# Kernel tuning notes

Hardware: AMD Instinct MI355X
Metric: run time of the kernel (lower is better)

Reference implementation:

```python
import jax, jax.numpy as jnp
import numpy as np

B, C, H, W = 32, 3, 224, 224
P = 16
D = 768
HEADS, DH = 12, 64
INNER = HEADS * DH          # 768
DEPTH = 12
NUM_CLASSES = 1000
NP_ = (H // P) * (W // P)   # 196 patches
N = NP_ + 1                 # with cls token
PATCH_DIM = C * P * P       # 768
EPS = 1e-5


def _ln(x, g, b):
    mu = jnp.mean(x, axis=-1, keepdims=True)
    var = jnp.var(x, axis=-1, keepdims=True)
    return (x - mu) * jax.lax.rsqrt(var + EPS) * g + b


def setup_inputs() -> dict:
    key = jax.random.key(0)
    ks = jax.random.split(key, 16)
    s = 0.02
    return {
        "img": jax.random.normal(ks[0], (B, C, H, W), jnp.float32),
        "sph_dist": jax.random.uniform(ks[1], (N, N), jnp.float32),
        "patch_ln_g": jnp.ones((PATCH_DIM,), jnp.float32),
        "patch_ln_b": jnp.zeros((PATCH_DIM,), jnp.float32),
        "W_patch": jax.random.normal(ks[2], (PATCH_DIM, D), jnp.float32) * s,
        "b_patch": jnp.zeros((D,), jnp.float32),
        "emb_ln_g": jnp.ones((D,), jnp.float32),
        "emb_ln_b": jnp.zeros((D,), jnp.float32),
        "pos_emb": jax.random.normal(ks[3], (1, N, D), jnp.float32),
        "cls_tok": jax.random.normal(ks[4], (1, 1, D), jnp.float32),
        "ln_g": jnp.ones((DEPTH, D), jnp.float32),
        "ln_b": jnp.zeros((DEPTH, D), jnp.float32),
        "W_qkv": jax.random.normal(ks[5], (DEPTH, D, 3 * INNER), jnp.float32) * s,
        "W_out": jax.random.normal(ks[6], (DEPTH, INNER, D), jnp.float32) * s,
        "b_out": jnp.zeros((DEPTH, D), jnp.float32),
        "final_ln_g": jnp.ones((D,), jnp.float32),
        "final_ln_b": jnp.zeros((D,), jnp.float32),
        "W_head": jax.random.normal(ks[7], (D, NUM_CLASSES), jnp.float32) * s,
        "b_head": jnp.zeros((NUM_CLASSES,), jnp.float32),
    }


def _patchify(img):
    b = img.shape[0]
    # 'b c (h p1) (w p2) -> b (h w) (p1 p2 c)'
    x = img.reshape(b, C, H // P, P, W // P, P)
    x = x.transpose(0, 2, 4, 3, 5, 1)  # b h w p1 p2 c
    return x.reshape(b, NP_, PATCH_DIM)


def _attn_layer(x, sph_dist, g, bln, Wqkv, Wout, bout):
    b, n, _ = x.shape
    xn = _ln(x, g, bln)
    qkv = xn @ Wqkv                                  # [b,n,3*inner]
    q, k, v = jnp.split(qkv, 3, axis=-1)
    def heads(t):
        return t.reshape(b, n, HEADS, DH).transpose(0, 2, 1, 3)  # b h n d
    q, k, v = heads(q), heads(k), heads(v)
    dots = jnp.einsum('bhid,bhjd->bhij', q, k) * (DH ** -0.5)
    dw = dots * (1.0 + sph_dist)                     # broadcast over b,h
    mu = jnp.mean(dw, axis=1, keepdims=True)
    sd = jnp.std(dw, axis=1, keepdims=True, ddof=1)  # torch.std is unbiased
    dw = (dw - mu) / sd
    attn = jax.nn.softmax(dw, axis=-1)
    o = jnp.einsum('bhij,bhjd->bhid', attn, v)
    o = o.transpose(0, 2, 1, 3).reshape(b, n, INNER)
    return o @ Wout + bout


def reference(img, sph_dist, patch_ln_g, patch_ln_b, W_patch, b_patch,
              emb_ln_g, emb_ln_b, pos_emb, cls_tok,
              ln_g, ln_b, W_qkv, W_out, b_out,
              final_ln_g, final_ln_b, W_head, b_head):
    b = img.shape[0]
    x = _patchify(img)
    x = _ln(x, patch_ln_g, patch_ln_b)
    x = x @ W_patch + b_patch
    x = _ln(x, emb_ln_g, emb_ln_b)                   # [b, 196, D]
    cls = jnp.broadcast_to(cls_tok, (b, 1, D))
    x = jnp.concatenate([cls, x], axis=1)            # [b, 197, D]
    x = x + pos_emb[:, :x.shape[1]]
    for i in range(DEPTH):
        x = _attn_layer(x, sph_dist, ln_g[i], ln_b[i], W_qkv[i], W_out[i], b_out[i]) + x
    x = _ln(x, final_ln_g, final_ln_b)
    x = x[:, 0]                                      # cls pooling
    return x @ W_head + b_head
```

## Files before the change

kernel.cpp:

```cpp
#include <hip/hip_runtime.h>
#include <math.h>

constexpr int Bc = 32, Cch = 3, Hh = 224, Ww = 224, Pp = 16;
constexpr int Dd = 768, NH = 12, DHd = 64, INNERc = 768;
constexpr int DEPTHc = 12, NCLS = 1000;
constexpr int NPc = 196, Nn = 197, PD = 768;
constexpr float EPSf = 1e-5f;

typedef _Float16 half_t;
typedef __attribute__((ext_vector_type(8))) _Float16 half8;
typedef __attribute__((ext_vector_type(4))) float f32x4;
typedef __attribute__((ext_vector_type(4))) unsigned int uint32x4;

__device__ __forceinline__ float wave_red_sum(float v) {
#pragma unroll
    for (int m = 32; m; m >>= 1) v += __shfl_xor(v, m);
    return v;
}

__device__ __forceinline__ void block_red2(float& s, float& s2, float* red) {
    s = wave_red_sum(s);
    s2 = wave_red_sum(s2);
    int wid = threadIdx.x >> 6, lane = threadIdx.x & 63;
    if (lane == 0) { red[wid] = s; red[4 + wid] = s2; }
    __syncthreads();
    s = red[0] + red[1] + red[2] + red[3];
    s2 = red[4] + red[5] + red[6] + red[7];
}

__global__ __launch_bounds__(256) void k_patch_ln(
        const float* __restrict__ img, const float* __restrict__ g,
        const float* __restrict__ bb, half_t* __restrict__ out) {
    int pid = blockIdx.x;
    int b = pid / NPc, n = pid % NPc;
    int ph = n / 14, pw = n % 14;
    int t = threadIdx.x;
    __shared__ float red[8];
    float v[3];
#pragma unroll
    for (int i = 0; i < 3; i++) {
        int d = t + i * 256;
        int c = d % 3, q = (d / 3) & 15, p = d / 48;
        v[i] = img[((long)(b * Cch + c) * Hh + ph * Pp + p) * Ww + pw * Pp + q];
    }
    float s = v[0] + v[1] + v[2];
    float s2 = v[0] * v[0] + v[1] * v[1] + v[2] * v[2];
    block_red2(s, s2, red);
    float mu = s * (1.f / PD);
    float var = s2 * (1.f / PD) - mu * mu;
    float r = rsqrtf(var + EPSf);
#pragma unroll
    for (int i = 0; i < 3; i++) {
        int d = t + i * 256;
        out[(long)pid * PD + d] = (half_t)((v[i] - mu) * r * g[d] + bb[d]);
    }
}

template <typename T>
__global__ __launch_bounds__(256) void k_ln(
        const float* __restrict__ in, const float* __restrict__ g,
        const float* __restrict__ bb, T* __restrict__ out,
        long in_stride, long out_stride) {
    long row = blockIdx.x;
    const float* ip = in + row * in_stride;
    T* op = out + row * out_stride;
    int t = threadIdx.x;
    __shared__ float red[8];
    float v[3];
#pragma unroll
    for (int i = 0; i < 3; i++) v[i] = ip[t + i * 256];
    float s = v[0] + v[1] + v[2];
    float s2 = v[0] * v[0] + v[1] * v[1] + v[2] * v[2];
    block_red2(s, s2, red);
    float mu = s * (1.f / Dd);
    float var = s2 * (1.f / Dd) - mu * mu;
    float r = rsqrtf(var + EPSf);
#pragma unroll
    for (int i = 0; i < 3; i++) {
        int d = t + i * 256;
        op[d] = (T)((v[i] - mu) * r * g[d] + bb[d]);
    }
}

__global__ __launch_bounds__(256) void k_embed(
        const float* __restrict__ tmp, const float* __restrict__ cls,
        const float* __restrict__ pos, const float* __restrict__ g,
        const float* __restrict__ bb, float* __restrict__ x) {
    int pid = blockIdx.x;
    int b = pid / Nn, n = pid % Nn;
    int t = threadIdx.x;
    float* xp = x + (long)pid * Dd;
    if (n == 0) {
#pragma unroll
        for (int i = 0; i < 3; i++) {
            int d = t + i * 256;
            xp[d] = cls[d] + pos[d];
        }
        return;
    }
    const float* ip = tmp + (long)(b * NPc + n - 1) * Dd;
    __shared__ float red[8];
    float v[3];
#pragma unroll
    for (int i = 0; i < 3; i++) v[i] = ip[t + i * 256];
    float s = v[0] + v[1] + v[2];
    float s2 = v[0] * v[0] + v[1] * v[1] + v[2] * v[2];
    block_red2(s, s2, red);
    float mu = s * (1.f / Dd);
    float var = s2 * (1.f / Dd) - mu * mu;
    float r = rsqrtf(var + EPSf);
#pragma unroll
    for (int i = 0; i < 3; i++) {
        int d = t + i * 256;
        xp[d] = (v[i] - mu) * r * g[d] + bb[d] + pos[(long)n * Dd + d];
    }
}

__global__ __launch_bounds__(256) void k_wprep(
        const float* __restrict__ W, half_t* __restrict__ Wt, int K, int N) {
    W += (long)blockIdx.z * K * N;
    Wt += (long)blockIdx.z * K * N;
    __shared__ float tile[32][33];
    int n = blockIdx.x * 32 + threadIdx.x;
    int k0 = blockIdx.y * 32;
#pragma unroll
    for (int i = 0; i < 4; i++)
        tile[threadIdx.y + i * 8][threadIdx.x] = W[(long)(k0 + threadIdx.y + i * 8) * N + n];
    __syncthreads();
    int kk = k0 + threadIdx.x;
#pragma unroll
    for (int i = 0; i < 4; i++)
        Wt[(long)(blockIdx.x * 32 + threadIdx.y + i * 8) * K + kk] =
            (half_t)tile[threadIdx.x][threadIdx.y + i * 8];
}

__global__ __launch_bounds__(256) void k_wprep_head(
        const float* __restrict__ W, half_t* __restrict__ Wt) {
    __shared__ float tile[32][33];
    int n = blockIdx.x * 32 + threadIdx.x;
    int k0 = blockIdx.y * 32;
#pragma unroll
    for (int i = 0; i < 4; i++)
        tile[threadIdx.y + i * 8][threadIdx.x] =
            (n < NCLS) ? W[(long)(k0 + threadIdx.y + i * 8) * NCLS + n] : 0.f;
    __syncthreads();
    int kk = k0 + threadIdx.x;
#pragma unroll
    for (int i = 0; i < 4; i++)
        Wt[(long)(blockIdx.x * 32 + threadIdx.y + i * 8) * Dd + kk] =
            (half_t)tile[threadIdx.x][threadIdx.y + i * 8];
}

__global__ __launch_bounds__(256) void k_head(
        const half_t* __restrict__ Ah, const half_t* __restrict__ Wh,
        const float* __restrict__ bias, float* __restrict__ out) {
    int idx = blockIdx.x * 256 + threadIdx.x;
    int row = idx >> 10, col = idx & 1023;
    if (col >= NCLS) return;
    const half_t* ap = Ah + (long)row * Dd;
    const half_t* wp = Wh + (long)col * Dd;
    float acc = 0.f;
#pragma unroll
    for (int k = 0; k < 96; k++) {
        half8 a = *(const half8*)&ap[k * 8];
        half8 w = *(const half8*)&wp[k * 8];
#pragma unroll
        for (int u = 0; u < 8; u++) acc += (float)a[u] * (float)w[u];
    }
    out[(long)row * NCLS + col] = acc + bias[col];
}

__device__ __forceinline__ half8 lds_frag(const uint32x4 (*L)[8], int row, int slot) {
    union { uint32x4 u; half8 h; } t;
    t.u = L[row][slot];
    return t.h;
}

__device__ __forceinline__ void gload16(const half_t* g, uint32x4* l) {
    __builtin_amdgcn_global_load_lds(
        (const __attribute__((address_space(1))) unsigned int*)g,
        (__attribute__((address_space(3))) unsigned int*)l,
        16, 0, 0);
}

template <int HASB, int HASR, typename CT, int OMODE>
__global__ __launch_bounds__(256, 2) void k_hgemm(
        const half_t* __restrict__ A, const half_t* __restrict__ Bt,
        const float* __restrict__ bias, const float* __restrict__ res,
        CT* __restrict__ C, CT* __restrict__ C1, half_t* __restrict__ Vt,
        int M, int N, int K) {
    __shared__ uint32x4 smem[2176];
    uint32x4 (*As)[8] = (uint32x4(*)[8])smem;
    uint32x4 (*Bs)[8] = (uint32x4(*)[8])(smem + 1024);
    const int tid = threadIdx.x;
    const int nwg = gridDim.x;
    const int q8 = nwg >> 3, r8 = nwg & 7;
    const int xc = blockIdx.x & 7, oo = blockIdx.x >> 3;
    const int tile = (xc < r8 ? xc * (q8 + 1) : r8 * (q8 + 1) + (xc - r8) * q8) + oo;
    const int gx = N >> 7;
    const int n0 = (tile % gx) * 128, m0 = (tile / gx) * 128;
    const int lane = tid & 63, w = tid >> 6;
    const int wrr = (w >> 1) * 64, wcc = (w & 1) * 64;
    const int lrow = lane & 15, lgrp = lane >> 4;

    int ldsOff[4];
    long gsA[4], gsB[4];
#pragma unroll
    for (int c = 0; c < 4; ++c) {
        int r = w * 32 + c * 8 + (lane >> 3);
        int chunk = (lane & 7) ^ (r & 7);
        ldsOff[c] = (w * 32 + c * 8) * 8;
        gsA[c] = (long)min(m0 + r, M - 1) * K + chunk * 8;
        gsB[c] = (long)(n0 + r) * K + chunk * 8;
    }

    f32x4 acc[4][4] = {};

#define STAGE(k0)                                         \
    {                                                     \
        _Pragma("unroll")                                 \
        for (int c = 0; c < 4; ++c) {                     \
            gload16(A + gsA[c] + (k0), smem + ldsOff[c]); \
            gload16(Bt + gsB[c] + (k0), smem + 1024 + ldsOff[c]); \
        }                                                 \
    }

    STAGE(0);
    __syncthreads();

    const int nst = K >> 6;
    for (int t = 0; t < nst; ++t) {
#pragma unroll
        for (int kh = 0; kh < 2; ++kh) {
            half8 af[4], bf[4];
#pragma unroll
            for (int i2 = 0; i2 < 4; ++i2) {
                int m = wrr + i2 * 16 + lrow;
                af[i2] = lds_frag(As, m, (kh * 4 + lgrp) ^ (m & 7));
                int n = wcc + i2 * 16 + lrow;
                bf[i2] = lds_frag(Bs, n, (kh * 4 + lgrp) ^ (n & 7));
            }
#pragma unroll
            for (int i2 = 0; i2 < 4; ++i2)
#pragma unroll
                for (int j2 = 0; j2 < 4; ++j2)
                    acc[i2][j2] = __builtin_amdgcn_mfma_f32_16x16x32_f16(af[i2], bf[j2], acc[i2][j2], 0, 0, 0);
        }
        if (t + 1 < nst) {
            __syncthreads();
            STAGE((t + 1) << 6);
            __syncthreads();
        }
    }
#undef STAGE

    if constexpr (sizeof(CT) == 2) {
        if constexpr (OMODE == 1) {
            if (n0 >= 1536) {
                __syncthreads();
                half_t* Cs = (half_t*)smem;
#pragma unroll
                for (int i2 = 0; i2 < 4; ++i2)
#pragma unroll
                    for (int j2 = 0; j2 < 4; ++j2) {
                        int colc = wcc + j2 * 16 + lrow;
#pragma unroll
                        for (int q = 0; q < 4; ++q) {
                            int r = wrr + i2 * 16 + lgrp * 4 + q;
                            Cs[colc * 136 + r] = (half_t)acc[i2][j2][q];
                        }
                    }
                __syncthreads();
                const int rr = tid & 127;
                const int cbase = (tid >> 7) * 64;
                int token = m0 + rr;
                bool ok = token < M;
                int b = 0, nn = 0;
                if (ok) { b = token / Nn; nn = token - b * Nn; }
#pragma unroll
                for (int cc = 0; cc < 64; ++cc) {
                    int c = cbase + cc;
                    int rem = n0 + c - 1536;
                    int h = rem >> 6, d = rem & 63;
                    if (ok)
                        Vt[((long)(b * NH + h) * 64 + d) * 224 + nn] = Cs[c * 136 + rr];
                }
                return;
            }
        }
        __syncthreads();
        half_t* Cs = (half_t*)smem;
#pragma unroll
        for (int i2 = 0; i2 < 4; ++i2)
#pragma unroll
            for (int j2 = 0; j2 < 4; ++j2) {
                int colc = wcc + j2 * 16 + lrow;
                float bv = HASB ? bias[n0 + colc] : 0.f;
#pragma unroll
                for (int q = 0; q < 4; ++q) {
                    int r = wrr + i2 * 16 + lgrp * 4 + q;
                    Cs[r * 136 + colc] = (half_t)(acc[i2][j2][q] + bv);
                }
            }
        __syncthreads();
#pragma unroll
        for (int it = 0; it < 8; ++it) {
            int idx = tid + it * 256;
            int row = idx >> 4, cu = idx & 15;
            int token = m0 + row;
            if (token < M) {
                uint32x4 val = *(const uint32x4*)(Cs + row * 136 + cu * 8);
                if constexpr (OMODE == 1) {
                    int gc = n0 + cu * 8;
                    int which = gc >= 768 ? 1 : 0;
                    int rem = gc - which * 768;
                    int h = rem >> 6, d = rem & 63;
                    int b = token / Nn, nn = token - b * Nn;
                    CT* dst = (which == 0 ? C : C1);
                    __builtin_nontemporal_store(val,
                        (uint32x4*)(dst + (((long)(b * NH + h) * Nn + nn) << 6) + d));
                } else {
                    __builtin_nontemporal_store(val,
                        (uint32x4*)(C + (long)token * N + n0 + cu * 8));
                }
            }
        }
    } else {
#pragma unroll
        for (int i2 = 0; i2 < 4; ++i2)
#pragma unroll
            for (int j2 = 0; j2 < 4; ++j2) {
                int colc = n0 + wcc + j2 * 16 + lrow;
                float bv = HASB ? bias[colc] : 0.f;
#pragma unroll
                for (int q = 0; q < 4; ++q) {
                    int r = m0 + wrr + i2 * 16 + lgrp * 4 + q;
                    if (r < M) {
                        float v = acc[i2][j2][q] + bv;
                        if (HASR) v += res[(long)r * N + colc];
                        __builtin_nontemporal_store(v, &C[(long)r * N + colc]);
                    }
                }
            }
    }
}

__global__ __launch_bounds__(256) void k_stats(
        const half_t* __restrict__ qh, const half_t* __restrict__ kh,
        f32x4* __restrict__ muT, f32x4* __restrict__ rsT) {
    const int blk = (blockIdx.x & 7) * 169 + (blockIdx.x >> 3);
    const int w = threadIdx.x >> 6, lane = threadIdx.x & 63;
    const int task = blk * 4 + w;
    const int b = task / 169, r = task % 169;
    const int it = r / 13, jt = r % 13;
    const int lrow = lane & 15, lg = lane >> 4;
    const int i0 = it * 16, j0 = jt * 16;
    const int arow = min(i0 + lrow, Nn - 1);
    const int jr = min(j0 + lrow, Nn - 1);
    const int hbase = b * NH;

    float sv[4] = {}, sq[4] = {};
#pragma unroll
    for (int h = 0; h < NH; h++) {
        const half_t* Qp = qh + ((long)(hbase + h) * Nn) * 64;
        const half_t* Kp = kh + ((long)(hbase + h) * Nn) * 64;
        half8 af0 = *(const half8*)&Qp[(long)arow * 64 + lg * 8];
        half8 af1 = *(const half8*)&Qp[(long)arow * 64 + 32 + lg * 8];
        half8 bf0 = *(const half8*)&Kp[(long)jr * 64 + lg * 8];
        half8 bf1 = *(const half8*)&Kp[(long)jr * 64 + 32 + lg * 8];
        f32x4 acc = {};
        acc = __builtin_amdgcn_mfma_f32_16x16x32_f16(af0, bf0, acc, 0, 0, 0);
        acc = __builtin_amdgcn_mfma_f32_16x16x32_f16(af1, bf1, acc, 0, 0, 0);
#pragma unroll
        for (int q = 0; q < 4; q++) { sv[q] += acc[q]; sq[q] += acc[q] * acc[q]; }
    }
    f32x4 muv, rsv;
#pragma unroll
    for (int q = 0; q < 4; q++) {
        float mu = sv[q] * (1.f / NH);
        float var = (sq[q] - sv[q] * mu) * (1.f / (NH - 1));
        muv[q] = mu;
        rsv[q] = rsqrtf(var);
    }
    long idx = ((long)(b * 13 + it) * 13 + jt) * 64 + lane;
    muT[idx] = muv;
    rsT[idx] = rsv;
}

__global__ __launch_bounds__(64) void k_attn2(
        const half_t* __restrict__ qh, const half_t* __restrict__ kh,
        const half_t* __restrict__ vt, const f32x4* __restrict__ muT,
        const f32x4* __restrict__ rsT, half_t* __restrict__ o) {
    __shared__ half_t PB[16][232];
    const int tile = (blockIdx.x & 7) * 624 + (blockIdx.x >> 3);
    const int bh = tile / 13, it = tile % 13;
    const int b = bh / NH, h = bh % NH;
    const int i0 = it * 16;
    const int lane = threadIdx.x;
    const int lrow = lane & 15, lg = lane >> 4;
    const int arow = min(i0 + lrow, Nn - 1);

    for (int idx = lane; idx < 16 * 12; idx += 64) {
        int rr = idx / 12, u = idx % 12;
        *(unsigned int*)&PB[rr][208 + u * 2] = 0u;
    }

    const half_t* Qp = qh + ((long)bh * Nn) * 64;
    const half_t* Kp = kh + ((long)bh * Nn) * 64;
    half8 af0 = *(const half8*)&Qp[(long)arow * 64 + lg * 8];
    half8 af1 = *(const half8*)&Qp[(long)arow * 64 + 32 + lg * 8];
    const f32x4* muB = muT + ((long)(b * 13 + it) * 13) * 64 + lane;
    const f32x4* rsB = rsT + ((long)(b * 13 + it) * 13) * 64 + lane;

    float ez[13][4];
    float mx[4] = {-1e30f, -1e30f, -1e30f, -1e30f};
#pragma unroll
    for (int jt = 0; jt < 13; jt++) {
        int jr = min(jt * 16 + lrow, Nn - 1);
        half8 bf0 = *(const half8*)&Kp[(long)jr * 64 + lg * 8];
        half8 bf1 = *(const half8*)&Kp[(long)jr * 64 + 32 + lg * 8];
        f32x4 acc = {};
        acc = __builtin_amdgcn_mfma_f32_16x16x32_f16(af0, bf0, acc, 0, 0, 0);
        acc = __builtin_amdgcn_mfma_f32_16x16x32_f16(af1, bf1, acc, 0, 0, 0);
        f32x4 mu4 = muB[jt * 64];
        f32x4 rs4 = rsB[jt * 64];
        bool joob = (jt * 16 + lrow) > Nn - 1;
#pragma unroll
        for (int q = 0; q < 4; q++) {
            float z = (acc[q] - mu4[q]) * rs4[q];
            if (joob) z = -1e30f;
            ez[jt][q] = z;
            mx[q] = fmaxf(mx[q], z);
        }
    }
#pragma unroll
    for (int st = 1; st <= 8; st <<= 1)
#pragma unroll
        for (int q = 0; q < 4; q++) mx[q] = fmaxf(mx[q], __shfl_xor(mx[q], st));
    float sm[4] = {0.f, 0.f, 0.f, 0.f};
#pragma unroll
    for (int jt = 0; jt < 13; jt++)
#pragma unroll
        for (int q = 0; q < 4; q++) {
            float e = __expf(ez[jt][q] - mx[q]);
            ez[jt][q] = e;
            sm[q] += e;
        }
#pragma unroll
    for (int st = 1; st <= 8; st <<= 1)
#pragma unroll
        for (int q = 0; q < 4; q++) sm[q] += __shfl_xor(sm[q], st);
    float inv[4];
#pragma unroll
    for (int q = 0; q < 4; q++) inv[q] = 1.f / sm[q];
#pragma unroll
    for (int jt = 0; jt < 13; jt++)
#pragma unroll
        for (int q = 0; q < 4; q++)
            PB[lg * 4 + q][jt * 16 + lrow] = (half_t)(ez[jt][q] * inv[q]);
    __syncthreads();

    const half_t* Vtp = vt + ((long)bh * 64) * 224;
#pragma unroll
    for (int dt = 0; dt < 4; dt++) {
        f32x4 oacc = {};
#pragma unroll
        for (int kt = 0; kt < 7; kt++) {
            half8 pa = *(const half8*)&PB[lrow][kt * 32 + lg * 8];
            half8 vb = *(const half8*)&Vtp[(long)(dt * 16 + lrow) * 224 + kt * 32 + lg * 8];
            oacc = __builtin_amdgcn_mfma_f32_16x16x32_f16(pa, vb, oacc, 0, 0, 0);
        }
#pragma unroll
        for (int q = 0; q < 4; q++) {
            int i = i0 + lg * 4 + q;
            if (i < Nn)
                o[((long)(b * Nn) + i) * INNERc + h * 64 + dt * 16 + lrow] = (half_t)oacc[q];
        }
    }
}

extern "C" void kernel_launch(void* const* d_in, const int* in_sizes, int n_in,
                              void* d_out, int out_size, void* d_ws, size_t ws_size,
                              hipStream_t stream) {
    const float* img     = (const float*)d_in[0];
    const float* patch_g = (const float*)d_in[2];
    const float* patch_b = (const float*)d_in[3];
    const float* W_patch = (const float*)d_in[4];
    const float* b_patch = (const float*)d_in[5];
    const float* emb_g   = (const float*)d_in[6];
    const float* emb_b   = (const float*)d_in[7];
    const float* pos     = (const float*)d_in[8];
    const float* cls     = (const float*)d_in[9];
    const float* ln_g    = (const float*)d_in[10];
    const float* ln_b    = (const float*)d_in[11];
    const float* W_qkv   = (const float*)d_in[12];
    const float* W_out   = (const float*)d_in[13];
    const float* b_out   = (const float*)d_in[14];
    const float* fin_g   = (const float*)d_in[15];
    const float* fin_b   = (const float*)d_in[16];
    const float* W_head  = (const float*)d_in[17];
    const float* b_head  = (const float*)d_in[18];
    float* out = (float*)d_out;

    const long SZ_XD  = (long)Bc * Nn * Dd;
    const long SZ_HD  = (long)Bc * NH * Nn * DHd;
    const long SZ_VT  = (long)Bc * NH * 64 * 224;
    const long SZ_TMP = (long)Bc * NPc * Dd;
    const long SZ_MU  = (long)Bc * 169 * 256 + 1024;

    float* x    = (float*)d_ws;
    float* tmp  = x + SZ_XD;
    float* muG  = tmp + SZ_TMP;
    float* rsG  = muG + SZ_MU;
    half_t* xh       = (half_t*)(rsG + SZ_MU);
    half_t* qhb      = xh + SZ_XD;
    half_t* khb      = qhb + SZ_HD;
    half_t* vtb      = khb + SZ_HD;
    half_t* clsh     = vtb + SZ_VT;
    half_t* wh_head  = clsh + 32 * Dd;
    half_t* wt_patch = wh_head + 1024 * Dd;
    half_t* wt_qkv   = wt_patch + (long)Dd * Dd;
    half_t* wt_out   = wt_qkv + (long)DEPTHc * 3 * INNERc * Dd;

    hipLaunchKernelGGL(k_wprep, dim3(Dd / 32, Dd / 32, 1), dim3(32, 8), 0, stream,
                       W_patch, wt_patch, Dd, Dd);
    hipLaunchKernelGGL(k_wprep, dim3(3 * INNERc / 32, Dd / 32, DEPTHc), dim3(32, 8), 0, stream,
                       W_qkv, wt_qkv, Dd, 3 * INNERc);
    hipLaunchKernelGGL(k_wprep, dim3(Dd / 32, Dd / 32, DEPTHc), dim3(32, 8), 0, stream,
                       W_out, wt_out, Dd, Dd);
    hipLaunchKernelGGL(k_wprep_head, dim3(32, 24), dim3(32, 8), 0, stream,
                       W_head, wh_head);

    hipLaunchKernelGGL(k_patch_ln, dim3(Bc * NPc), dim3(256), 0, stream,
                       img, patch_g, patch_b, xh);
    hipLaunchKernelGGL((k_hgemm<1, 0, float, 0>), dim3(6 * 49), dim3(256), 0, stream,
                       xh, wt_patch, b_patch, nullptr,
                       tmp, nullptr, nullptr, Bc * NPc, Dd, Dd);
    hipLaunchKernelGGL(k_embed, dim3(Bc * Nn), dim3(256), 0, stream,
                       tmp, cls, pos, emb_g, emb_b, x);

    const int Mrows = Bc * Nn;
    for (int l = 0; l < DEPTHc; l++) {
        const float* g  = ln_g + (long)l * Dd;
        const float* bb = ln_b + (long)l * Dd;
        const half_t* Wq = wt_qkv + (long)l * 3 * INNERc * Dd;
        const half_t* Wo = wt_out + (long)l * Dd * Dd;
        const float* bo = b_out + (long)l * Dd;
        hipLaunchKernelGGL((k_ln<half_t>), dim3(Mrows), dim3(256), 0, stream,
                           x, g, bb, xh, (long)Dd, (long)Dd);
        hipLaunchKernelGGL((k_hgemm<0, 0, half_t, 1>), dim3(18 * 50), dim3(256), 0, stream,
                           xh, Wq, nullptr, nullptr,
                           qhb, khb, vtb, Mrows, 3 * INNERc, Dd);
        hipLaunchKernelGGL(k_stats, dim3(1352), dim3(256), 0, stream,
                           qhb, khb, (f32x4*)muG, (f32x4*)rsG);
        hipLaunchKernelGGL(k_attn2, dim3(4992), dim3(64), 0, stream,
                           qhb, khb, vtb, (const f32x4*)muG, (const f32x4*)rsG, xh);
        hipLaunchKernelGGL((k_hgemm<1, 1, float, 0>), dim3(6 * 50), dim3(256), 0, stream,
                           xh, Wo, bo, x,
                           x, nullptr, nullptr, Mrows, Dd, Dd);
    }
    hipLaunchKernelGGL((k_ln<half_t>), dim3(Bc), dim3(256), 0, stream,
                       x, fin_g, fin_b, clsh, (long)Nn * Dd, (long)Dd);
    hipLaunchKernelGGL(k_head, dim3(128), dim3(256), 0, stream,
                       clsh, wh_head, b_head, out);
}
```

Before: 1.702 ms.

## Split attention stats and softmax work across two waves per tile

k_stats now splits the 12-head sum for each tile across two waves (6 heads each) and combines the partial sums through shared memory, doubling the grid. k_attn2 uses two waves per 16-row tile: each wave computes about half of the key tiles, the waves share row max and sum through LDS, and each wave computes two of the four output d-tiles. The aim is more parallelism and less serial latency per wave. The cost is extra barriers, LDS traffic and some idle lanes from the uneven 7/6 key-tile split.

Measured after the change: 1.670 ms. About the same (-1.9%).

```diff
diff --git a/kernel.cpp b/kernel.cpp
--- a/kernel.cpp
+++ b/kernel.cpp
@@ -348,20 +348,22 @@
 __global__ __launch_bounds__(256) void k_stats(
         const half_t* __restrict__ qh, const half_t* __restrict__ kh,
         f32x4* __restrict__ muT, f32x4* __restrict__ rsT) {
-    const int blk = (blockIdx.x & 7) * 169 + (blockIdx.x >> 3);
+    __shared__ f32x4 redv[2][64], redq[2][64];
+    const int blk = (blockIdx.x & 7) * 338 + (blockIdx.x >> 3);
     const int w = threadIdx.x >> 6, lane = threadIdx.x & 63;
-    const int task = blk * 4 + w;
+    const int ti = w >> 1, hh2 = w & 1;
+    const int task = blk * 2 + ti;
     const int b = task / 169, r = task % 169;
     const int it = r / 13, jt = r % 13;
     const int lrow = lane & 15, lg = lane >> 4;
     const int i0 = it * 16, j0 = jt * 16;
     const int arow = min(i0 + lrow, Nn - 1);
     const int jr = min(j0 + lrow, Nn - 1);
-    const int hbase = b * NH;
+    const int hbase = b * NH + hh2 * 6;
 
     float sv[4] = {}, sq[4] = {};
 #pragma unroll
-    for (int h = 0; h < NH; h++) {
+    for (int h = 0; h < 6; h++) {
         const half_t* Qp = qh + ((long)(hbase + h) * Nn) * 64;
         const half_t* Kp = kh + ((long)(hbase + h) * Nn) * 64;
         half8 af0 = *(const half8*)&Qp[(long)arow * 64 + lg * 8];
@@ -374,35 +376,54 @@
 #pragma unroll
         for (int q = 0; q < 4; q++) { sv[q] += acc[q]; sq[q] += acc[q] * acc[q]; }
     }
-    f32x4 muv, rsv;
-#pragma unroll
-    for (int q = 0; q < 4; q++) {
-        float mu = sv[q] * (1.f / NH);
-        float var = (sq[q] - sv[q] * mu) * (1.f / (NH - 1));
-        muv[q] = mu;
-        rsv[q] = rsqrtf(var);
-    }
-    long idx = ((long)(b * 13 + it) * 13 + jt) * 64 + lane;
-    muT[idx] = muv;
-    rsT[idx] = rsv;
-}
-
-__global__ __launch_bounds__(64) void k_attn2(
+    if (hh2 == 1) {
+        f32x4 a, b2;
+#pragma unroll
+        for (int q = 0; q < 4; q++) { a[q] = sv[q]; b2[q] = sq[q]; }
+        redv[ti][lane] = a;
+        redq[ti][lane] = b2;
+    }
+    __syncthreads();
+    if (hh2 == 0) {
+        f32x4 a = redv[ti][lane], b2 = redq[ti][lane];
+        f32x4 muv, rsv;
+#pragma unroll
+        for (int q = 0; q < 4; q++) {
+            float svt = sv[q] + a[q];
+            float sqt = sq[q] + b2[q];
+            float mu = svt * (1.f / NH);
+            float var = (sqt - svt * mu) * (1.f / (NH - 1));
+            muv[q] = mu;
+            rsv[q] = rsqrtf(var);
+        }
+        long idx = ((long)(b * 13 + it) * 13 + jt) * 64 + lane;
+        muT[idx] = muv;
+        rsT[idx] = rsv;
+    }
+}
+
+__global__ __launch_bounds__(128) void k_attn2(
         const half_t* __restrict__ qh, const half_t* __restrict__ kh,
         const half_t* __restrict__ vt, const f32x4* __restrict__ muT,
         const f32x4* __restrict__ rsT, half_t* __restrict__ o) {
     __shared__ half_t PB[16][232];
+    __shared__ float xmx[2][16], xsm[2][16];
     const int tile = (blockIdx.x & 7) * 624 + (blockIdx.x >> 3);
     const int bh = tile / 13, it = tile % 13;
     const int b = bh / NH, h = bh % NH;
     const int i0 = it * 16;
-    const int lane = threadIdx.x;
+    const int tid = threadIdx.x;
+    const int wv = tid >> 6, lane = tid & 63;
     const int lrow = lane & 15, lg = lane >> 4;
     const int arow = min(i0 + lrow, Nn - 1);
-
-    for (int idx = lane; idx < 16 * 12; idx += 64) {
-        int rr = idx / 12, u = idx % 12;
-        *(unsigned int*)&PB[rr][208 + u * 2] = 0u;
+    const int jtbase = wv * 7;
+    const int njt = 7 - wv;
+
+    if (wv == 0) {
+        for (int idx = lane; idx < 128; idx += 64) {
+            int rr = idx >> 3, u = idx & 7;
+            *(unsigned int*)&PB[rr][208 + u * 2] = 0u;
+        }
     }
 
     const half_t* Qp = qh + ((long)bh * Nn) * 64;
@@ -412,57 +433,82 @@
     const f32x4* muB = muT + ((long)(b * 13 + it) * 13) * 64 + lane;
     const f32x4* rsB = rsT + ((long)(b * 13 + it) * 13) * 64 + lane;
 
-    float ez[13][4];
+    float ez[7][4];
     float mx[4] = {-1e30f, -1e30f, -1e30f, -1e30f};
 #pragma unroll
-    for (int jt = 0; jt < 13; jt++) {
-        int jr = min(jt * 16 + lrow, Nn - 1);
-        half8 bf0 = *(const half8*)&Kp[(long)jr * 64 + lg * 8];
-        half8 bf1 = *(const half8*)&Kp[(long)jr * 64 + 32 + lg * 8];
-        f32x4 acc = {};
-        acc = __builtin_amdgcn_mfma_f32_16x16x32_f16(af0, bf0, acc, 0, 0, 0);
-        acc = __builtin_amdgcn_mfma_f32_16x16x32_f16(af1, bf1, acc, 0, 0, 0);
-        f32x4 mu4 = muB[jt * 64];
-        f32x4 rs4 = rsB[jt * 64];
-        bool joob = (jt * 16 + lrow) > Nn - 1;
-#pragma unroll
-        for (int q = 0; q < 4; q++) {
-            float z = (acc[q] - mu4[q]) * rs4[q];
-            if (joob) z = -1e30f;
-            ez[jt][q] = z;
-            mx[q] = fmaxf(mx[q], z);
+    for (int jj = 0; jj < 7; jj++) {
+        if (jj < njt) {
+            int jt = jtbase + jj;
+            int jr = min(jt * 16 + lrow, Nn - 1);
+            half8 bf0 = *(const half8*)&Kp[(long)jr * 64 + lg * 8];
+            half8 bf1 = *(const half8*)&Kp[(long)jr * 64 + 32 + lg * 8];
+            f32x4 acc = {};
+            acc = __builtin_amdgcn_mfma_f32_16x16x32_f16(af0, bf0, acc, 0, 0, 0);
+            acc = __builtin_amdgcn_mfma_f32_16x16x32_f16(af1, bf1, acc, 0, 0, 0);
+            f32x4 mu4 = muB[jt * 64];
+            f32x4 rs4 = rsB[jt * 64];
+            bool joob = (jt * 16 + lrow) > Nn - 1;
+#pragma unroll
+            for (int q = 0; q < 4; q++) {
+                float z = (acc[q] - mu4[q]) * rs4[q];
+                if (joob) z = -1e30f;
+                ez[jj][q] = z;
+                mx[q] = fmaxf(mx[q], z);
+            }
         }
     }
 #pragma unroll
     for (int st = 1; st <= 8; st <<= 1)
 #pragma unroll
         for (int q = 0; q < 4; q++) mx[q] = fmaxf(mx[q], __shfl_xor(mx[q], st));
+    if (lrow == 0) {
+#pragma unroll
+        for (int q = 0; q < 4; q++) xmx[wv][lg * 4 + q] = mx[q];
+    }
+    __syncthreads();
+    float cmx[4];
+#pragma unroll
+    for (int q = 0; q < 4; q++)
+        cmx[q] = fmaxf(xmx[0][lg * 4 + q], xmx[1][lg * 4 + q]);
     float sm[4] = {0.f, 0.f, 0.f, 0.f};
 #pragma unroll
-    for (int jt = 0; jt < 13; jt++)
-#pragma unroll
-        for (int q = 0; q < 4; q++) {
-            float e = __expf(ez[jt][q] - mx[q]);
-            ez[jt][q] = e;
-            sm[q] += e;
-        }
+    for (int jj = 0; jj < 7; jj++) {
+        if (jj < njt) {
+#pragma unroll
+            for (int q = 0; q < 4; q++) {
+                float e = __expf(ez[jj][q] - cmx[q]);
+                ez[jj][q] = e;
+                sm[q] += e;
+            }
+        }
+    }
 #pragma unroll
     for (int st = 1; st <= 8; st <<= 1)
 #pragma unroll
         for (int q = 0; q < 4; q++) sm[q] += __shfl_xor(sm[q], st);
+    if (lrow == 0) {
+#pragma unroll
+        for (int q = 0; q < 4; q++) xsm[wv][lg * 4 + q] = sm[q];
+    }
+    __syncthreads();
     float inv[4];
 #pragma unroll
-    for (int q = 0; q < 4; q++) inv[q] = 1.f / sm[q];
-#pragma unroll
-    for (int jt = 0; jt < 13; jt++)
-#pragma unroll
-        for (int q = 0; q < 4; q++)
-            PB[lg * 4 + q][jt * 16 + lrow] = (half_t)(ez[jt][q] * inv[q]);
+    for (int q = 0; q < 4; q++)
+        inv[q] = 1.f / (xsm[0][lg * 4 + q] + xsm[1][lg * 4 + q]);
+#pragma unroll
+    for (int jj = 0; jj < 7; jj++) {
+        if (jj < njt) {
+#pragma unroll
+            for (int q = 0; q < 4; q++)
+                PB[lg * 4 + q][(jtbase + jj) * 16 + lrow] = (half_t)(ez[jj][q] * inv[q]);
+        }
+    }
     __syncthreads();
 
     const half_t* Vtp = vt + ((long)bh * 64) * 224;
 #pragma unroll
-    for (int dt = 0; dt < 4; dt++) {
+    for (int dd = 0; dd < 2; dd++) {
+        int dt = wv * 2 + dd;
         f32x4 oacc = {};
 #pragma unroll
         for (int kt = 0; kt < 7; kt++) {
@@ -551,9 +597,9 @@
         hipLaunchKernelGGL((k_hgemm<0, 0, half_t, 1>), dim3(18 * 50), dim3(256), 0, stream,
                            xh, Wq, nullptr, nullptr,
                            qhb, khb, vtb, Mrows, 3 * INNERc, Dd);
-        hipLaunchKernelGGL(k_stats, dim3(1352), dim3(256), 0, stream,
+        hipLaunchKernelGGL(k_stats, dim3(2704), dim3(256), 0, stream,
                            qhb, khb, (f32x4*)muG, (f32x4*)rsG);
-        hipLaunchKernelGGL(k_attn2, dim3(4992), dim3(64), 0, stream,
+        hipLaunchKernelGGL(k_attn2, dim3(4992), dim3(128), 0, stream,
                            qhb, khb, vtb, (const f32x4*)muG, (const f32x4*)rsG, xh);
         hipLaunchKernelGGL((k_hgemm<1, 1, float, 0>), dim3(6 * 50), dim3(256), 0, stream,
                            xh, Wo, bo, x,
```
